# Kernel tuning notes

Hardware: AMD Instinct MI355X
Metric: run time of the kernel (lower is better)

The kernel has to match this reference:

```python
import jax, jax.numpy as jnp
import numpy as np

# ProjectorConfig defaults
MIN_SPEECH_FRAMES = 1.0
MAX_SPEECH_EXPAND = 3.0
TAIL_HOLD_UNITS = 2
BOUNDARY_COMMIT_THRESHOLD = 0.45

B, U = 4096, 2048


def setup_inputs() -> dict:
    key = jax.random.key(0)
    ks = jax.random.split(key, 10)
    # ragged prefix mask: random visible length per row (faithful to streaming use)
    lengths = jax.random.randint(ks[0], (B,), 1, U + 1)
    unit_mask = (jnp.arange(U)[None, :] < lengths[:, None]).astype(jnp.float32)
    dur_anchor_src = jax.random.uniform(ks[1], (B, U), jnp.float32) * 20.0
    dur_logratio_unit = jax.random.normal(ks[2], (B, U), jnp.float32) * 0.3
    pause_weight_unit = jax.random.uniform(ks[3], (B, U), jnp.float32)
    boundary_latent = jax.random.uniform(ks[4], (B, U), jnp.float32)
    speech_budget_win = jax.random.uniform(ks[5], (B, 1), jnp.float32) * float(U) * 10.0
    pause_budget_win = jax.random.uniform(ks[6], (B, 1), jnp.float32) * float(U)
    open_run_mask = jax.random.bernoulli(ks[7], 0.1, (B, U)).astype(jnp.int32)
    return {
        "dur_anchor_src": dur_anchor_src,
        "unit_mask": unit_mask,
        "speech_budget_win": speech_budget_win,
        "pause_budget_win": pause_budget_win,
        "dur_logratio_unit": dur_logratio_unit,
        "pause_weight_unit": pause_weight_unit,
        "boundary_latent": boundary_latent,
        "phase_ptr": jnp.zeros((B,), jnp.float32),
        "backlog": jnp.zeros((B,), jnp.float32),
        "clock_delta": jnp.zeros((B,), jnp.float32),
        "commit_frontier": jnp.zeros((B,), jnp.int32),
        "open_run_mask": open_run_mask,
    }


def reference(dur_anchor_src, unit_mask, speech_budget_win, pause_budget_win,
              dur_logratio_unit, pause_weight_unit, boundary_latent,
              phase_ptr, backlog, clock_delta, commit_frontier, open_run_mask):
    b, u = unit_mask.shape

    # ---- _project_speech ----
    anchor = jnp.maximum(dur_anchor_src, MIN_SPEECH_FRAMES)
    base = anchor * jnp.exp(dur_logratio_unit)
    speech = jnp.maximum(jnp.minimum(base, anchor * MAX_SPEECH_EXPAND), MIN_SPEECH_FRAMES) * unit_mask
    total = jnp.maximum((speech * unit_mask).sum(axis=1, keepdims=True), 1e-6)
    speech = speech * (speech_budget_win / total) * unit_mask

    # ---- _project_pause ----
    scores = jnp.maximum(pause_weight_unit, 0.0) * (0.5 + boundary_latent) * unit_mask
    score_total = scores.sum(axis=1, keepdims=True)
    fallback = unit_mask / jnp.maximum(unit_mask.sum(axis=1, keepdims=True), 1.0)
    weights = jnp.where(score_total > 0, scores / jnp.maximum(score_total, 1e-6), fallback)
    pause = weights * pause_budget_win

    effective = (speech + pause) * unit_mask

    # ---- _compute_commit_frontier (vectorized) ----
    visible = unit_mask.sum(axis=1).astype(jnp.int32)                 # active_len [B]
    idx = jnp.arange(u, dtype=jnp.int32)[None, :]
    open_vis = (open_run_mask > 0) & (idx < visible[:, None])
    has_open = open_vis.any(axis=1)
    first_open = jnp.argmax(open_vis, axis=1).astype(jnp.int32)
    closed_prefix = jnp.where(has_open, first_open, visible)          # leading closed run
    release_cap = jnp.maximum(visible - TAIL_HOLD_UNITS, 0)
    candidate = jnp.minimum(release_cap, closed_prefix)
    prev = commit_frontier.astype(jnp.int32)
    b_idx = jnp.clip(candidate - 1, 0, u - 1)
    b_val = jnp.take_along_axis(boundary_latent, b_idx[:, None], axis=1)[:, 0]
    soft = (candidate > 0) & (candidate < visible) & (b_val < BOUNDARY_COMMIT_THRESHOLD)
    candidate = jnp.where(soft, jnp.maximum(prev, candidate - 1), candidate)
    commit = jnp.maximum(prev, candidate)

    # ---- _advance_state (prefix sums instead of python loops) ----
    zeros_col = jnp.zeros((b, 1), effective.dtype)
    cs_eff = jnp.concatenate([zeros_col, jnp.cumsum(effective, axis=1)], axis=1)
    cs_src = jnp.concatenate([zeros_col, jnp.cumsum(dur_anchor_src, axis=1)], axis=1)
    take = lambda cs, i: jnp.take_along_axis(cs, i[:, None], axis=1)[:, 0]
    exec_prefix = take(cs_eff, commit) - take(cs_eff, prev)
    src_prefix = take(cs_src, commit) - take(cs_src, prev)
    adv = commit > prev
    delta = exec_prefix - src_prefix
    next_clock = jnp.where(adv, clock_delta + delta, clock_delta)
    next_backlog = jnp.where(adv, jnp.maximum(next_clock, 0.0), backlog)
    visible_total = jnp.maximum(effective.sum(axis=1), 1.0)
    next_phase = jnp.where(adv, jnp.clip(phase_ptr + exec_prefix / visible_total, 0.0, 1.0), phase_ptr)

    return (speech, pause, effective, commit, next_phase, next_backlog, next_clock)
```

## Files before the change

### kernel.cpp

```cpp
#include <hip/hip_runtime.h>
#include <climits>


constexpr int UNITS = 2048;
constexpr int BLOCK = 256;
constexpr int EPT = UNITS / BLOCK;

typedef float f32x4 __attribute__((ext_vector_type(4)));

static __device__ __forceinline__ float waveSum(float v) {
#pragma unroll
  for (int m = 1; m < 64; m <<= 1) v += __shfl_xor(v, m, 64);
  return v;
}
static __device__ __forceinline__ int waveMin(int v) {
#pragma unroll
  for (int m = 1; m < 64; m <<= 1) v = min(v, __shfl_xor(v, m, 64));
  return v;
}

__global__ __launch_bounds__(BLOCK, 4) void rhythm_kernel(
    const float* __restrict__ dur_anchor,
    const float* __restrict__ unit_mask,
    const float* __restrict__ speech_budget,
    const float* __restrict__ pause_budget,
    const float* __restrict__ dur_logratio,
    const float* __restrict__ pause_weight,
    const float* __restrict__ boundary,
    const float* __restrict__ phase_ptr,
    const float* __restrict__ backlog,
    const float* __restrict__ clock_delta,
    const int*   __restrict__ commit_front,
    const int*   __restrict__ open_run,
    float* __restrict__ out,
    int B) {
  const int row = blockIdx.x;
  const int t = threadIdx.x;
  const size_t base = (size_t)row * UNITS;

  const int prev = commit_front[row];
  const float sb = speech_budget[row];
  const float pb = pause_budget[row];
  const float pp = phase_ptr[row];
  const float bl = backlog[row];
  const float cd = clock_delta[row];

  float sv_sr[EPT];
  float sv_sc[EPT];
  float sum_sr = 0.f, sum_sc = 0.f, sum_m = 0.f;
  int min_open = INT_MAX;

#pragma unroll
  for (int c = 0; c < EPT / 4; ++c) {
    const int e0 = c * (BLOCK * 4) + 4 * t;
    const float4 a4 = *(const float4*)(dur_anchor   + base + e0);
    const float4 m4 = *(const float4*)(unit_mask    + base + e0);
    const float4 l4 = *(const float4*)(dur_logratio + base + e0);
    const float4 p4 = *(const float4*)(pause_weight + base + e0);
    const float4 b4 = *(const float4*)(boundary     + base + e0);
    const int4   o4 = *(const int4*)(open_run       + base + e0);
    const float av[4] = {a4.x, a4.y, a4.z, a4.w};
    const float mv[4] = {m4.x, m4.y, m4.z, m4.w};
    const float lv[4] = {l4.x, l4.y, l4.z, l4.w};
    const float pv[4] = {p4.x, p4.y, p4.z, p4.w};
    const float bv[4] = {b4.x, b4.y, b4.z, b4.w};
    const int   ov[4] = {o4.x, o4.y, o4.z, o4.w};
#pragma unroll
    for (int j = 0; j < 4; ++j) {
      const int k = c * 4 + j;
      const float m = mv[j];
      const float a = fmaxf(av[j], 1.0f);
      const float bse = a * __expf(lv[j]);
      const float sr = fmaxf(fminf(bse, 3.0f * a), 1.0f) * m;
      const float sc = fmaxf(pv[j], 0.0f) * (0.5f + bv[j]) * m;
      sv_sr[k] = sr;
      sv_sc[k] = sc;
      sum_sr += sr;
      sum_sc += sc;
      sum_m += m;
      if (ov[j] > 0 && m > 0.5f) min_open = min(min_open, e0 + j);
    }
  }

  const int wv = t >> 6, ln = t & 63;
  __shared__ float sf[3][4];
  __shared__ int si[4];
  __shared__ float sg[2][4];

  const float r0 = waveSum(sum_sr);
  const float r1 = waveSum(sum_sc);
  const float r2 = waveSum(sum_m);
  const int ri = waveMin(min_open);
  if (ln == 0) { sf[0][wv] = r0; sf[1][wv] = r1; sf[2][wv] = r2; si[wv] = ri; }
  __syncthreads();

  const float ts = sf[0][0] + sf[0][1] + sf[0][2] + sf[0][3];
  const float tc = sf[1][0] + sf[1][1] + sf[1][2] + sf[1][3];
  const float tm = sf[2][0] + sf[2][1] + sf[2][2] + sf[2][3];
  const int mo = min(min(si[0], si[1]), min(si[2], si[3]));

  const int visible = (int)(tm + 0.5f);
  const int closed = (mo == INT_MAX) ? visible : mo;
  const int relcap = max(visible - 2, 0);
  int cand = min(relcap, closed);
  const int bidx = min(max(cand - 1, 0), UNITS - 1);
  const float bval = boundary[base + bidx];
  if (cand > 0 && cand < visible && bval < 0.45f)
    cand = max(prev, cand - 1);
  const int commit = max(prev, cand);

  const float sscale = sb / fmaxf(ts, 1e-6f);
  const bool usefb = !(tc > 0.0f);
  const float pscale = pb / fmaxf(tc, 1e-6f);
  const float fbw = pb / fmaxf(tm, 1.0f);
  const float eff_tot = usefb ? (sscale * ts + fbw * tm) : (sscale * ts + pscale * tc);

  float src_rng = 0.f;
  for (int i = prev + t; i < commit; i += BLOCK) src_rng += dur_anchor[base + i];

  float* __restrict__ out_speech = out;
  float* __restrict__ out_pause  = out + (size_t)B * UNITS;
  float* __restrict__ out_eff    = out + 2 * (size_t)B * UNITS;

  float eff_rng = 0.f;
#pragma unroll
  for (int c = 0; c < EPT / 4; ++c) {
    const int e0 = c * (BLOCK * 4) + 4 * t;
    f32x4 s4, q4, e4;
#pragma unroll
    for (int j = 0; j < 4; ++j) {
      const int k = c * 4 + j;
      const int idx = e0 + j;
      const float sr = sv_sr[k];
      const float m = (sr != 0.0f) ? 1.0f : 0.0f;
      const float speech = sr * sscale;
      const float pause = usefb ? (m * fbw) : (sv_sc[k] * pscale);
      const float eff = (speech + pause) * m;
      s4[j] = speech;
      q4[j] = pause;
      e4[j] = eff;
      const bool inr = (idx >= prev) && (idx < commit);
      eff_rng += inr ? eff : 0.f;
    }
    __builtin_nontemporal_store(s4, (f32x4*)(out_speech + base + e0));
    __builtin_nontemporal_store(q4, (f32x4*)(out_pause + base + e0));
    __builtin_nontemporal_store(e4, (f32x4*)(out_eff + base + e0));
  }

  const float q0 = waveSum(eff_rng);
  const float q1 = waveSum(src_rng);
  if (ln == 0) { sg[0][wv] = q0; sg[1][wv] = q1; }
  __syncthreads();

  if (t == 0) {
    const float execp = sg[0][0] + sg[0][1] + sg[0][2] + sg[0][3];
    const float srcp  = sg[1][0] + sg[1][1] + sg[1][2] + sg[1][3];
    const bool adv = commit > prev;
    const float nclock = adv ? (cd + (execp - srcp)) : cd;
    const float nback = adv ? fmaxf(nclock, 0.0f) : bl;
    const float vt = fmaxf(eff_tot, 1.0f);
    const float nphase =
        adv ? fminf(fmaxf(pp + execp / vt, 0.0f), 1.0f) : pp;
    const size_t o = 3 * (size_t)B * UNITS;
    out[o + row] = (float)commit;
    out[o + (size_t)B + row] = nphase;
    out[o + 2 * (size_t)B + row] = nback;
    out[o + 3 * (size_t)B + row] = nclock;
  }
}

extern "C" void kernel_launch(void* const* d_in, const int* in_sizes, int n_in,
                              void* d_out, int out_size, void* d_ws, size_t ws_size,
                              hipStream_t stream) {
  const int B = in_sizes[7];
  rhythm_kernel<<<dim3(B), dim3(BLOCK), 0, stream>>>(
      (const float*)d_in[0],
      (const float*)d_in[1],
      (const float*)d_in[2],
      (const float*)d_in[3],
      (const float*)d_in[4],
      (const float*)d_in[5],
      (const float*)d_in[6],
      (const float*)d_in[7],
      (const float*)d_in[8],
      (const float*)d_in[9],
      (const int*)d_in[10],
      (const int*)d_in[11],
      (float*)d_out, B);
}
```

Before: 265.6 us.

## Map one row per wavefront instead of one row per block

Each 64-lane wavefront now processes a whole row (32 elements per lane), with four rows per 256-thread block. The shared-memory cross-wave reductions and both __syncthreads barriers are replaced by wave-level butterfly reductions. This removes block synchronization, but each lane now keeps 64 values in registers (sv_sr, sv_sc), which raises register pressure and may reduce occupancy under launch_bounds(256,4). The serial src range loop also steps by 64 instead of 256, so it runs more iterations per lane.

Result: slower. 277.7 us (+4.6%).

```diff
diff --git a/kernel.cpp b/kernel.cpp
--- a/kernel.cpp
+++ b/kernel.cpp
@@ -4,16 +4,17 @@
 
 constexpr int UNITS = 2048;
 constexpr int BLOCK = 256;
-constexpr int EPT = UNITS / BLOCK;
+constexpr int ELEMS = UNITS / 64;
+constexpr int CHUNKS = ELEMS / 4;
 
 typedef float f32x4 __attribute__((ext_vector_type(4)));
 
-static __device__ __forceinline__ float waveSum(float v) {
+static __device__ __forceinline__ float bflySum(float v) {
 #pragma unroll
   for (int m = 1; m < 64; m <<= 1) v += __shfl_xor(v, m, 64);
   return v;
 }
-static __device__ __forceinline__ int waveMin(int v) {
+static __device__ __forceinline__ int bflyMin(int v) {
 #pragma unroll
   for (int m = 1; m < 64; m <<= 1) v = min(v, __shfl_xor(v, m, 64));
   return v;
@@ -34,8 +35,10 @@
     const int*   __restrict__ open_run,
     float* __restrict__ out,
     int B) {
-  const int row = blockIdx.x;
-  const int t = threadIdx.x;
+  const int w = threadIdx.x >> 6;
+  const int ln = threadIdx.x & 63;
+  const int row = blockIdx.x * 4 + w;
+  if (row >= B) return;
   const size_t base = (size_t)row * UNITS;
 
   const int prev = commit_front[row];
@@ -45,14 +48,14 @@
   const float bl = backlog[row];
   const float cd = clock_delta[row];
 
-  float sv_sr[EPT];
-  float sv_sc[EPT];
+  float sv_sr[ELEMS];
+  float sv_sc[ELEMS];
   float sum_sr = 0.f, sum_sc = 0.f, sum_m = 0.f;
   int min_open = INT_MAX;
 
 #pragma unroll
-  for (int c = 0; c < EPT / 4; ++c) {
-    const int e0 = c * (BLOCK * 4) + 4 * t;
+  for (int c = 0; c < CHUNKS; ++c) {
+    const int e0 = c * 256 + 4 * ln;
     const float4 a4 = *(const float4*)(dur_anchor   + base + e0);
     const float4 m4 = *(const float4*)(unit_mask    + base + e0);
     const float4 l4 = *(const float4*)(dur_logratio + base + e0);
@@ -82,22 +85,10 @@
     }
   }
 
-  const int wv = t >> 6, ln = t & 63;
-  __shared__ float sf[3][4];
-  __shared__ int si[4];
-  __shared__ float sg[2][4];
-
-  const float r0 = waveSum(sum_sr);
-  const float r1 = waveSum(sum_sc);
-  const float r2 = waveSum(sum_m);
-  const int ri = waveMin(min_open);
-  if (ln == 0) { sf[0][wv] = r0; sf[1][wv] = r1; sf[2][wv] = r2; si[wv] = ri; }
-  __syncthreads();
-
-  const float ts = sf[0][0] + sf[0][1] + sf[0][2] + sf[0][3];
-  const float tc = sf[1][0] + sf[1][1] + sf[1][2] + sf[1][3];
-  const float tm = sf[2][0] + sf[2][1] + sf[2][2] + sf[2][3];
-  const int mo = min(min(si[0], si[1]), min(si[2], si[3]));
+  const float ts = bflySum(sum_sr);
+  const float tc = bflySum(sum_sc);
+  const float tm = bflySum(sum_m);
+  const int mo = bflyMin(min_open);
 
   const int visible = (int)(tm + 0.5f);
   const int closed = (mo == INT_MAX) ? visible : mo;
@@ -116,7 +107,7 @@
   const float eff_tot = usefb ? (sscale * ts + fbw * tm) : (sscale * ts + pscale * tc);
 
   float src_rng = 0.f;
-  for (int i = prev + t; i < commit; i += BLOCK) src_rng += dur_anchor[base + i];
+  for (int i = prev + ln; i < commit; i += 64) src_rng += dur_anchor[base + i];
 
   float* __restrict__ out_speech = out;
   float* __restrict__ out_pause  = out + (size_t)B * UNITS;
@@ -124,8 +115,8 @@
 
   float eff_rng = 0.f;
 #pragma unroll
-  for (int c = 0; c < EPT / 4; ++c) {
-    const int e0 = c * (BLOCK * 4) + 4 * t;
+  for (int c = 0; c < CHUNKS; ++c) {
+    const int e0 = c * 256 + 4 * ln;
     f32x4 s4, q4, e4;
 #pragma unroll
     for (int j = 0; j < 4; ++j) {
@@ -147,14 +138,10 @@
     __builtin_nontemporal_store(e4, (f32x4*)(out_eff + base + e0));
   }
 
-  const float q0 = waveSum(eff_rng);
-  const float q1 = waveSum(src_rng);
-  if (ln == 0) { sg[0][wv] = q0; sg[1][wv] = q1; }
-  __syncthreads();
+  const float execp = bflySum(eff_rng);
+  const float srcp = bflySum(src_rng);
 
-  if (t == 0) {
-    const float execp = sg[0][0] + sg[0][1] + sg[0][2] + sg[0][3];
-    const float srcp  = sg[1][0] + sg[1][1] + sg[1][2] + sg[1][3];
+  if (ln == 0) {
     const bool adv = commit > prev;
     const float nclock = adv ? (cd + (execp - srcp)) : cd;
     const float nback = adv ? fmaxf(nclock, 0.0f) : bl;
@@ -173,7 +160,7 @@
                               void* d_out, int out_size, void* d_ws, size_t ws_size,
                               hipStream_t stream) {
   const int B = in_sizes[7];
-  rhythm_kernel<<<dim3(B), dim3(BLOCK), 0, stream>>>(
+  rhythm_kernel<<<dim3((B + 3) / 4), dim3(BLOCK), 0, stream>>>(
       (const float*)d_in[0],
       (const float*)d_in[1],
       (const float*)d_in[2],
```
